# Kernel optimization log

Hardware: AMD Instinct MI355X
Metric: run time of the kernel (lower is better)

Reference implementation:

```python
import jax, jax.numpy as jnp
import numpy as np

N, D = 6144, 128
NUM_CLASSES, NUM_BATCHES = 20, 5
MIN_T, MAX_T = 0.1, 1.0
TEMP_BATCH = 0.5  # fixed per-batch-key temperature set in __init__
EPS = 1e-8        # F.cosine_similarity eps


def _class_weights(labels, n):
    c = jnp.bincount(labels, length=n).astype(jnp.float32)
    w = 1.0 / c
    return w / w.sum()


def setup_inputs() -> dict:
    key = jax.random.key(0)
    k1, k2, k3 = jax.random.split(key, 3)
    x = jax.random.normal(k1, (N, D), dtype=jnp.float32)
    targets = jax.random.randint(k2, (N,), 0, NUM_CLASSES)
    batch0 = jax.random.randint(k3, (N,), 0, NUM_BATCHES)
    return {
        "input": x,
        "temperature": jnp.float32(0.25),
        "weight_target": _class_weights(targets, NUM_CLASSES),
        "weight_batch0": _class_weights(batch0, NUM_BATCHES),
        "targets": targets,
        "batch0": batch0,
    }


def _snn_losses(S, pos_mask, neg_mask):
    # S: [N,N] exp-similarities; masks include/exclude self consistently with torch code
    diag = jnp.diagonal(S)
    pos_sum = jnp.einsum('ij,ij->i', S, pos_mask.astype(S.dtype)) - diag  # self is in pos_mask
    neg_sum = jnp.einsum('ij,ij->i', S, neg_mask.astype(S.dtype))
    cnt_pos = pos_mask.sum(axis=1)  # includes self
    cnt_neg = neg_mask.sum(axis=1)
    valid = (cnt_pos >= 2) & (cnt_neg >= 1)
    pos_safe = jnp.where(valid, pos_sum, 1.0)
    neg_safe = jnp.where(valid, neg_sum, 1.0)
    loss_i = -jnp.log(pos_safe / (pos_safe + neg_safe))
    return loss_i, valid


def _weighted_class_sum(loss_i, valid, labels, weights, num_segments):
    lsum = jax.ops.segment_sum(jnp.where(valid, loss_i, 0.0), labels, num_segments=num_segments)
    cnt = jax.ops.segment_sum(valid.astype(jnp.float32), labels, num_segments=num_segments)
    mean = lsum / jnp.maximum(cnt, 1.0)
    return jnp.sum(jnp.where(cnt > 0, mean * weights, 0.0))


def reference(input, temperature, weight_target, weight_batch0, targets, batch0):
    t = jnp.clip(temperature, MIN_T, MAX_T)
    norms = jnp.maximum(jnp.linalg.norm(input, axis=1, keepdims=True), EPS)
    xn = input / norms
    sim = xn @ xn.T  # [N, N] cosine similarity

    same_t = targets[:, None] == targets[None, :]

    # ----- target (cell-type) SNN loss -----
    S_t = jnp.exp(sim / t)
    loss_i, valid = _snn_losses(S_t, same_t, ~same_t)
    loss_target = _weighted_class_sum(loss_i, valid, targets, weight_target, NUM_CLASSES)

    # ----- batch-effect loss (one batch key), reciprocal of -log -----
    S_b = jnp.exp(sim / TEMP_BATCH)
    same_b = batch0[:, None] == batch0[None, :]
    pos_mask = same_t & same_b
    neg_mask = same_t & (~same_b)
    loss_bi, valid_b = _snn_losses(S_b, pos_mask, neg_mask)
    loss_bi = jnp.where(valid_b, 1.0 / jnp.where(valid_b, loss_bi, 1.0), 0.0)
    loss_batch = _weighted_class_sum(loss_bi, valid_b, batch0, weight_batch0, NUM_BATCHES)
    # single batch key -> mean over batch keys is just loss_batch

    return 0.9 * loss_target + 0.1 * loss_batch
```

## Files before the change

kernel.cpp:

```cpp
#include <hip/hip_runtime.h>
#include <hip/hip_bf16.h>
#include <math.h>

#define NN 6144
#define DD 128
#define NCLS 20
#define NBATCH 5
#define NB 48
#define NPAIR (NB * (NB + 1) / 2)

typedef float f32x4 __attribute__((ext_vector_type(4)));
typedef short bf16x8 __attribute__((ext_vector_type(8)));

#define SOFF (NN * DD / 2)
#define AOFF (SOFF + 4 * NN)
#define COFF (AOFF + 50)

#define GLD16(gp, lp)                                                          \
    __builtin_amdgcn_global_load_lds(                                          \
        (const __attribute__((address_space(1))) void*)(gp),                   \
        (__attribute__((address_space(3))) void*)(lp), 16, 0, 0)

__global__ __launch_bounds__(256) void k_prep(const float* __restrict__ x,
                                              float* __restrict__ ws) {
    const int t = threadIdx.x;
    if (blockIdx.x < 24) {
        float4 z = {0.f, 0.f, 0.f, 0.f};
        *(float4*)(ws + SOFF + blockIdx.x * 1024 + t * 4) = z;
    } else if (blockIdx.x == 24) {
        if (t < 51) ws[AOFF + t] = 0.0f;
    }
    const int lane = t & 63;
    const int row = blockIdx.x * 4 + (t >> 6);
    float2 v = *(const float2*)(x + row * DD + 2 * lane);
    float s = v.x * v.x + v.y * v.y;
#pragma unroll
    for (int m = 1; m < 64; m <<= 1) s += __shfl_xor(s, m, 64);
    float rinv = 1.0f / fmaxf(sqrtf(s), 1e-8f);
    __hip_bfloat16 h0 = __float2bfloat16(v.x * rinv);
    __hip_bfloat16 h1 = __float2bfloat16(v.y * rinv);
    ushort2 u;
    u.x = *(ushort*)&h0;
    u.y = *(ushort*)&h1;
    ushort* xnb = (ushort*)ws;
    *(ushort2*)(xnb + row * DD + 2 * lane) = u;
}

#define RED16(v)                                                      \
    {                                                                 \
        float s0 = up3 ? v[0] : v[2], k0 = up3 ? v[2] : v[0];         \
        float s1 = up3 ? v[1] : v[3], k1 = up3 ? v[3] : v[1];         \
        v[0] = k0 + __shfl_xor(s0, 8, 64);                            \
        v[1] = k1 + __shfl_xor(s1, 8, 64);                            \
        float s2 = up2 ? v[0] : v[1], k2 = up2 ? v[1] : v[0];         \
        v[0] = k2 + __shfl_xor(s2, 4, 64);                            \
        v[0] += __shfl_xor(v[0], 2, 64);                              \
        v[0] += __shfl_xor(v[0], 1, 64);                              \
    }

#define RED4(v)                                                       \
    {                                                                 \
        float s0 = q1 ? v[0] : v[2], k0 = q1 ? v[2] : v[0];           \
        float s1 = q1 ? v[1] : v[3], k1 = q1 ? v[3] : v[1];           \
        v[0] = k0 + __shfl_xor(s0, 32, 64);                           \
        v[1] = k1 + __shfl_xor(s1, 32, 64);                           \
        float s2 = q0 ? v[0] : v[1], k2 = q0 ? v[1] : v[0];           \
        v[0] = k2 + __shfl_xor(s2, 16, 64);                           \
    }

__global__ __launch_bounds__(256) void k_main(const float* __restrict__ temp,
                                              const int* __restrict__ tg,
                                              const int* __restrict__ bt,
                                              float* __restrict__ ws) {
    __shared__ __align__(16) char smem[32768];
    __shared__ int tgA[128], btA[128], tgB[128], btB[128];

    char* tAc = smem;
    char* tBc = smem + 16384;
    float* sRowF = (float*)smem;
    float* sColF = (float*)(smem + 4096);

    const ushort* xnb = (const ushort*)ws;
    float* PT = ws + SOFF;
    float* TT = PT + NN;
    float* PB = PT + 2 * NN;
    float* TB = PT + 3 * NN;

    int bi = 0, rem = blockIdx.x;
    while (rem >= NB - bi) { rem -= NB - bi; ++bi; }
    const int bj = bi + rem;
    const int I = bi * 128, J = bj * 128;
    const bool isDiag = (bi == bj);

    const int t = threadIdx.x;
    const int w = t >> 6;
    const int lane = t & 63;
    const int tx16 = lane & 15;
    const int quad = lane >> 4;
    const int rowBase = (w >> 1) * 64;
    const int colBase = (w & 1) * 64;

    const float tc = fminf(fmaxf(temp[0], 0.1f), 1.0f);
    const float c1 = 1.4426950408889634f / tc;
    const float c2 = 2.8853900817779268f;

    if (t < 128) { tgA[t] = tg[I + t]; btA[t] = bt[I + t]; }
    else { int u2 = t - 128; tgB[u2] = tg[J + u2]; btB[u2] = bt[J + u2]; }

    const int rloc = lane >> 3;
    const int csw = (lane & 7) ^ rloc;

    f32x4 acc[4][4];
#pragma unroll
    for (int mt = 0; mt < 4; ++mt)
#pragma unroll
        for (int nt = 0; nt < 4; ++nt) acc[mt][nt] = (f32x4){0.f, 0.f, 0.f, 0.f};

    for (int kc = 0; kc < 2; ++kc) {
        if (kc) __syncthreads();
        {
            const ushort* gA = xnb + (size_t)(I + 32 * w + rloc) * DD + kc * 64 + csw * 8;
            const ushort* gB = xnb + (size_t)(J + 32 * w + rloc) * DD + kc * 64 + csw * 8;
            char* lA = tAc + (32 * w) * 128;
            char* lB = tBc + (32 * w) * 128;
#pragma unroll
            for (int q = 0; q < 4; ++q) {
                GLD16(gA + q * 8 * DD, lA + q * 1024);
                GLD16(gB + q * 8 * DD, lB + q * 1024);
            }
        }
        __syncthreads();
#pragma unroll
        for (int ks = 0; ks < 2; ++ks) {
            bf16x8 a[4], b[4];
            const int ca = (ks * 4 + quad) ^ (tx16 & 7);
#pragma unroll
            for (int mt = 0; mt < 4; ++mt)
                a[mt] = *(const bf16x8*)(tAc + (rowBase + 16 * mt + tx16) * 128 + ca * 16);
#pragma unroll
            for (int nt = 0; nt < 4; ++nt)
                b[nt] = *(const bf16x8*)(tBc + (colBase + 16 * nt + tx16) * 128 + ca * 16);
#pragma unroll
            for (int mt = 0; mt < 4; ++mt)
#pragma unroll
                for (int nt = 0; nt < 4; ++nt)
                    acc[mt][nt] = __builtin_amdgcn_mfma_f32_16x16x32_bf16(
                        a[mt], b[nt], acc[mt][nt], 0, 0, 0);
        }
    }

    __syncthreads();

    float cPT[4] = {0}, cTT[4] = {0}, cPB[4] = {0}, cTB[4] = {0};
    int tjv[4], bjv[4];
#pragma unroll
    for (int nt = 0; nt < 4; ++nt) {
        int jl = colBase + 16 * nt + tx16;
        tjv[nt] = tgB[jl];
        bjv[nt] = btB[jl];
    }
    const bool up3 = (tx16 >> 3) & 1;
    const bool up2 = (tx16 >> 2) & 1;
    const int pOwn = tx16 >> 2;

#pragma unroll
    for (int mt = 0; mt < 4; ++mt) {
        float rPT[4] = {0}, rTT[4] = {0}, rPB[4] = {0}, rTB[4] = {0};
        int til[4], bil[4];
#pragma unroll
        for (int p = 0; p < 4; ++p) {
            int il = rowBase + 16 * mt + 4 * quad + p;
            til[p] = tgA[il];
            bil[p] = btA[il];
        }
        if (isDiag) {
#pragma unroll
            for (int nt = 0; nt < 4; ++nt) {
                const int jl = colBase + 16 * nt + tx16;
#pragma unroll
                for (int p = 0; p < 4; ++p) {
                    const int il = rowBase + 16 * mt + 4 * quad + p;
                    float s = acc[mt][nt][p];
                    float et = __builtin_amdgcn_exp2f(c1 * s);
                    float eb = __builtin_amdgcn_exp2f(c2 * s);
                    bool nd = (il != jl);
                    bool st = (til[p] == tjv[nt]) && nd;
                    bool sb = (bil[p] == bjv[nt]);
                    rTT[p] += nd ? et : 0.f;
                    rPT[p] += st ? et : 0.f;
                    rTB[p] += st ? eb : 0.f;
                    rPB[p] += (st && sb) ? eb : 0.f;
                }
            }
        } else {
#pragma unroll
            for (int nt = 0; nt < 4; ++nt) {
#pragma unroll
                for (int p = 0; p < 4; ++p) {
                    float s = acc[mt][nt][p];
                    float et = __builtin_amdgcn_exp2f(c1 * s);
                    float eb = __builtin_amdgcn_exp2f(c2 * s);
                    bool st = (til[p] == tjv[nt]);
                    bool sb = (bil[p] == bjv[nt]);
                    float etp = st ? et : 0.f;
                    float ebp = st ? eb : 0.f;
                    float ebb = (st && sb) ? eb : 0.f;
                    rTT[p] += et;
                    rPT[p] += etp;
                    rTB[p] += ebp;
                    rPB[p] += ebb;
                    cTT[nt] += et;
                    cPT[nt] += etp;
                    cTB[nt] += ebp;
                    cPB[nt] += ebb;
                }
            }
        }
        RED16(rPT);
        RED16(rTT);
        RED16(rPB);
        RED16(rTB);
        if ((tx16 & 3) == 0) {
            int il = rowBase + 16 * mt + 4 * quad + pOwn;
            int rep = (w & 1) * 512;
            sRowF[rep + 0 * 128 + il] = rPT[0];
            sRowF[rep + 1 * 128 + il] = rTT[0];
            sRowF[rep + 2 * 128 + il] = rPB[0];
            sRowF[rep + 3 * 128 + il] = rTB[0];
        }
    }
    if (!isDiag) {
        const bool q1 = (quad >> 1) & 1;
        const bool q0 = quad & 1;
        RED4(cPT);
        RED4(cTT);
        RED4(cPB);
        RED4(cTB);
        int cl = colBase + 16 * quad + tx16;
        int rep = (w >> 1) * 512;
        sColF[rep + 0 * 128 + cl] = cPT[0];
        sColF[rep + 1 * 128 + cl] = cTT[0];
        sColF[rep + 2 * 128 + cl] = cPB[0];
        sColF[rep + 3 * 128 + cl] = cTB[0];
    }

    __syncthreads();
    if (t < 128) {
        int gi = I + t;
        atomicAdd(&PT[gi], sRowF[0 * 128 + t] + sRowF[512 + 0 * 128 + t]);
        atomicAdd(&TT[gi], sRowF[1 * 128 + t] + sRowF[512 + 1 * 128 + t]);
        atomicAdd(&PB[gi], sRowF[2 * 128 + t] + sRowF[512 + 2 * 128 + t]);
        atomicAdd(&TB[gi], sRowF[3 * 128 + t] + sRowF[512 + 3 * 128 + t]);
    } else if (!isDiag) {
        int u2 = t - 128;
        int gj = J + u2;
        atomicAdd(&PT[gj], sColF[0 * 128 + u2] + sColF[512 + 0 * 128 + u2]);
        atomicAdd(&TT[gj], sColF[1 * 128 + u2] + sColF[512 + 1 * 128 + u2]);
        atomicAdd(&PB[gj], sColF[2 * 128 + u2] + sColF[512 + 2 * 128 + u2]);
        atomicAdd(&TB[gj], sColF[3 * 128 + u2] + sColF[512 + 3 * 128 + u2]);
    }
}

__global__ __launch_bounds__(256) void k_fin(const int* __restrict__ tg,
                                             const int* __restrict__ bt,
                                             const float* __restrict__ wt,
                                             const float* __restrict__ wb,
                                             float* __restrict__ ws,
                                             float* __restrict__ out) {
    __shared__ int hh[NCLS + NCLS * NBATCH];
    __shared__ float ph[4][52];
    __shared__ int lastFlag;
    const int t = threadIdx.x;
    const int wv = t >> 6;
    if (t < NCLS + NCLS * NBATCH) hh[t] = 0;
    if (t < 52 * 4) ((float*)ph)[t] = 0.0f;
    __syncthreads();
    for (int i = t; i < NN; i += 256) {
        int c = tg[i], b = bt[i];
        atomicAdd(&hh[c], 1);
        atomicAdd(&hh[NCLS + c * NBATCH + b], 1);
    }
    __syncthreads();
    const float* PT = ws + SOFF;
    const float* TT = PT + NN;
    const float* PB = PT + 2 * NN;
    const float* TB = PT + 3 * NN;
    {
        const int i = blockIdx.x * 256 + t;
        float pt = PT[i], tt = TT[i], pb = PB[i], tb = TB[i];
        int ti = tg[i], bi = bt[i];
        int cp = hh[ti];
        int cpb = hh[NCLS + ti * NBATCH + bi];
        if (cp >= 2 && (NN - cp) >= 1) {
            float loss = logf(tt / pt);
            atomicAdd(&ph[wv][ti], loss);
            atomicAdd(&ph[wv][20 + ti], 1.0f);
        }
        if (cpb >= 2 && (cp - cpb) >= 1) {
            float lb = logf(tb / pb);
            atomicAdd(&ph[wv][40 + bi], 1.0f / lb);
            atomicAdd(&ph[wv][45 + bi], 1.0f);
        }
    }
    __syncthreads();
    if (t < 50) {
        float s = ph[0][t] + ph[1][t] + ph[2][t] + ph[3][t];
        atomicAdd(&ws[AOFF + t], s);
    }
    __syncthreads();
    if (t == 0) {
        __threadfence();
        lastFlag = (atomicAdd((int*)(ws + COFF), 1) == 23) ? 1 : 0;
    }
    __syncthreads();
    if (lastFlag) {
        __threadfence();
        if (t < 64) {
            const float* acc = ws + AOFF;
            float term = 0.0f;
            if (t < NCLS) {
                float cnt = acc[NCLS + t];
                if (cnt > 0.f) term = 0.9f * (acc[t] / cnt) * wt[t];
            } else if (t >= 32 && t < 32 + NBATCH) {
                int b = t - 32;
                float cnt = acc[2 * NCLS + NBATCH + b];
                if (cnt > 0.f) term = 0.1f * (acc[2 * NCLS + b] / cnt) * wb[b];
            }
#pragma unroll
            for (int m = 1; m < 64; m <<= 1) term += __shfl_xor(term, m, 64);
            if (t == 0) out[0] = term;
        }
    }
}

extern "C" void kernel_launch(void* const* d_in, const int* in_sizes, int n_in,
                              void* d_out, int out_size, void* d_ws, size_t ws_size,
                              hipStream_t stream) {
    const float* x    = (const float*)d_in[0];
    const float* temp = (const float*)d_in[1];
    const float* wt   = (const float*)d_in[2];
    const float* wb   = (const float*)d_in[3];
    const int*   tg   = (const int*)d_in[4];
    const int*   bt   = (const int*)d_in[5];
    float* out = (float*)d_out;
    float* ws = (float*)d_ws;

    k_prep<<<NN / 4, 256, 0, stream>>>(x, ws);
    k_main<<<NPAIR, 256, 0, stream>>>(temp, tg, bt, ws);
    k_fin<<<24, 256, 0, stream>>>(tg, bt, wt, wb, ws, out);
}
```

Baseline: 99.81 us.

## Give each wave its own 64x64 triangular tile, dropping block syncs and LDS reductions

Changes the decomposition from one 128x128 upper-triangle tile per 256-thread block to one independent 64x64 tile per wave. Each wave loads its own A/B panels into a private LDS region, uses waitcnt instead of block barriers, and reads labels with wave shuffles. Row and column partial sums now go straight to global atomics, with no LDS staging. This removes block-level synchronisation and cross-wave LDS traffic. In exchange, each element of x is loaded about twice as often, global atomics increase, and LDS use per block doubles to 64KB, which may lower occupancy.

```diff
diff --git a/kernel.cpp b/kernel.cpp
--- a/kernel.cpp
+++ b/kernel.cpp
@@ -6,8 +6,8 @@
 #define DD 128
 #define NCLS 20
 #define NBATCH 5
-#define NB 48
-#define NPAIR (NB * (NB + 1) / 2)
+#define NT 96
+#define NWT (NT * (NT + 1) / 2)
 
 typedef float f32x4 __attribute__((ext_vector_type(4)));
 typedef short bf16x8 __attribute__((ext_vector_type(8)));
@@ -20,6 +20,19 @@
     __builtin_amdgcn_global_load_lds(                                          \
         (const __attribute__((address_space(1))) void*)(gp),                   \
         (__attribute__((address_space(3))) void*)(lp), 16, 0, 0)
+
+#define WAIT_VM0()                                 \
+    do {                                           \
+        __builtin_amdgcn_sched_barrier(0);         \
+        __builtin_amdgcn_s_waitcnt(0x0F70);        \
+        __builtin_amdgcn_sched_barrier(0);         \
+    } while (0)
+#define WAIT_LGKM0()                               \
+    do {                                           \
+        __builtin_amdgcn_sched_barrier(0);         \
+        __builtin_amdgcn_s_waitcnt(0xC07F);        \
+        __builtin_amdgcn_sched_barrier(0);         \
+    } while (0)
 
 __global__ __launch_bounds__(256) void k_prep(const float* __restrict__ x,
                                               float* __restrict__ ws) {
@@ -72,13 +85,7 @@
                                               const int* __restrict__ tg,
                                               const int* __restrict__ bt,
                                               float* __restrict__ ws) {
-    __shared__ __align__(16) char smem[32768];
-    __shared__ int tgA[128], btA[128], tgB[128], btB[128];
-
-    char* tAc = smem;
-    char* tBc = smem + 16384;
-    float* sRowF = (float*)smem;
-    float* sColF = (float*)(smem + 4096);
+    __shared__ __align__(16) char smem[65536];
 
     const ushort* xnb = (const ushort*)ws;
     float* PT = ws + SOFF;
@@ -86,26 +93,31 @@
     float* PB = PT + 2 * NN;
     float* TB = PT + 3 * NN;
 
-    int bi = 0, rem = blockIdx.x;
-    while (rem >= NB - bi) { rem -= NB - bi; ++bi; }
-    const int bj = bi + rem;
-    const int I = bi * 128, J = bj * 128;
-    const bool isDiag = (bi == bj);
-
     const int t = threadIdx.x;
     const int w = t >> 6;
     const int lane = t & 63;
     const int tx16 = lane & 15;
     const int quad = lane >> 4;
-    const int rowBase = (w >> 1) * 64;
-    const int colBase = (w & 1) * 64;
+
+    const int idx = blockIdx.x * 4 + w;
+    int ti = (int)((2 * NT + 1 - sqrtf((float)((2 * NT + 1) * (2 * NT + 1) - 8 * idx))) * 0.5f);
+    if (ti < 0) ti = 0;
+    if (ti > NT - 1) ti = NT - 1;
+    while (ti > 0 && ti * (2 * NT - ti + 1) / 2 > idx) --ti;
+    while ((ti + 1) * (2 * NT - ti) / 2 <= idx) ++ti;
+    const int tj = ti + (idx - ti * (2 * NT - ti + 1) / 2);
+    const int IA = ti * 64, JB = tj * 64;
+    const bool isDiag = (ti == tj);
+
+    char* lA = smem + w * 16384;
+    char* lB = lA + 8192;
 
     const float tc = fminf(fmaxf(temp[0], 0.1f), 1.0f);
     const float c1 = 1.4426950408889634f / tc;
     const float c2 = 2.8853900817779268f;
 
-    if (t < 128) { tgA[t] = tg[I + t]; btA[t] = bt[I + t]; }
-    else { int u2 = t - 128; tgB[u2] = tg[J + u2]; btB[u2] = bt[J + u2]; }
+    const int tgi = tg[IA + lane], bti = bt[IA + lane];
+    const int tgj = tg[JB + lane], btj = bt[JB + lane];
 
     const int rloc = lane >> 3;
     const int csw = (lane & 7) ^ rloc;
@@ -117,29 +129,27 @@
         for (int nt = 0; nt < 4; ++nt) acc[mt][nt] = (f32x4){0.f, 0.f, 0.f, 0.f};
 
     for (int kc = 0; kc < 2; ++kc) {
-        if (kc) __syncthreads();
+        if (kc) WAIT_LGKM0();
         {
-            const ushort* gA = xnb + (size_t)(I + 32 * w + rloc) * DD + kc * 64 + csw * 8;
-            const ushort* gB = xnb + (size_t)(J + 32 * w + rloc) * DD + kc * 64 + csw * 8;
-            char* lA = tAc + (32 * w) * 128;
-            char* lB = tBc + (32 * w) * 128;
-#pragma unroll
-            for (int q = 0; q < 4; ++q) {
-                GLD16(gA + q * 8 * DD, lA + q * 1024);
-                GLD16(gB + q * 8 * DD, lB + q * 1024);
+            const ushort* gA = xnb + (size_t)(IA + rloc) * DD + kc * 64 + csw * 8;
+            const ushort* gB = xnb + (size_t)(JB + rloc) * DD + kc * 64 + csw * 8;
+#pragma unroll
+            for (int q = 0; q < 8; ++q) {
+                GLD16(gA + (size_t)q * 8 * DD, lA + q * 1024);
+                GLD16(gB + (size_t)q * 8 * DD, lB + q * 1024);
             }
         }
-        __syncthreads();
+        WAIT_VM0();
 #pragma unroll
         for (int ks = 0; ks < 2; ++ks) {
             bf16x8 a[4], b[4];
             const int ca = (ks * 4 + quad) ^ (tx16 & 7);
 #pragma unroll
             for (int mt = 0; mt < 4; ++mt)
-                a[mt] = *(const bf16x8*)(tAc + (rowBase + 16 * mt + tx16) * 128 + ca * 16);
+                a[mt] = *(const bf16x8*)(lA + (16 * mt + tx16) * 128 + ca * 16);
 #pragma unroll
             for (int nt = 0; nt < 4; ++nt)
-                b[nt] = *(const bf16x8*)(tBc + (colBase + 16 * nt + tx16) * 128 + ca * 16);
+                b[nt] = *(const bf16x8*)(lB + (16 * nt + tx16) * 128 + ca * 16);
 #pragma unroll
             for (int mt = 0; mt < 4; ++mt)
 #pragma unroll
@@ -149,15 +159,12 @@
         }
     }
 
-    __syncthreads();
-
     float cPT[4] = {0}, cTT[4] = {0}, cPB[4] = {0}, cTB[4] = {0};
     int tjv[4], bjv[4];
 #pragma unroll
     for (int nt = 0; nt < 4; ++nt) {
-        int jl = colBase + 16 * nt + tx16;
-        tjv[nt] = tgB[jl];
-        bjv[nt] = btB[jl];
+        tjv[nt] = __shfl(tgj, 16 * nt + tx16, 64);
+        bjv[nt] = __shfl(btj, 16 * nt + tx16, 64);
     }
     const bool up3 = (tx16 >> 3) & 1;
     const bool up2 = (tx16 >> 2) & 1;
@@ -169,17 +176,16 @@
         int til[4], bil[4];
 #pragma unroll
         for (int p = 0; p < 4; ++p) {
-            int il = rowBase + 16 * mt + 4 * quad + p;
-            til[p] = tgA[il];
-            bil[p] = btA[il];
+            til[p] = __shfl(tgi, 16 * mt + 4 * quad + p, 64);
+            bil[p] = __shfl(bti, 16 * mt + 4 * quad + p, 64);
         }
         if (isDiag) {
 #pragma unroll
             for (int nt = 0; nt < 4; ++nt) {
-                const int jl = colBase + 16 * nt + tx16;
+                const int jl = 16 * nt + tx16;
 #pragma unroll
                 for (int p = 0; p < 4; ++p) {
-                    const int il = rowBase + 16 * mt + 4 * quad + p;
+                    const int il = 16 * mt + 4 * quad + p;
                     float s = acc[mt][nt][p];
                     float et = __builtin_amdgcn_exp2f(c1 * s);
                     float eb = __builtin_amdgcn_exp2f(c2 * s);
@@ -221,12 +227,11 @@
         RED16(rPB);
         RED16(rTB);
         if ((tx16 & 3) == 0) {
-            int il = rowBase + 16 * mt + 4 * quad + pOwn;
-            int rep = (w & 1) * 512;
-            sRowF[rep + 0 * 128 + il] = rPT[0];
-            sRowF[rep + 1 * 128 + il] = rTT[0];
-            sRowF[rep + 2 * 128 + il] = rPB[0];
-            sRowF[rep + 3 * 128 + il] = rTB[0];
+            int gi = IA + 16 * mt + 4 * quad + pOwn;
+            atomicAdd(&PT[gi], rPT[0]);
+            atomicAdd(&TT[gi], rTT[0]);
+            atomicAdd(&PB[gi], rPB[0]);
+            atomicAdd(&TB[gi], rTB[0]);
         }
     }
     if (!isDiag) {
@@ -236,28 +241,11 @@
         RED4(cTT);
         RED4(cPB);
         RED4(cTB);
-        int cl = colBase + 16 * quad + tx16;
-        int rep = (w >> 1) * 512;
-        sColF[rep + 0 * 128 + cl] = cPT[0];
-        sColF[rep + 1 * 128 + cl] = cTT[0];
-        sColF[rep + 2 * 128 + cl] = cPB[0];
-        sColF[rep + 3 * 128 + cl] = cTB[0];
-    }
-
-    __syncthreads();
-    if (t < 128) {
-        int gi = I + t;
-        atomicAdd(&PT[gi], sRowF[0 * 128 + t] + sRowF[512 + 0 * 128 + t]);
-        atomicAdd(&TT[gi], sRowF[1 * 128 + t] + sRowF[512 + 1 * 128 + t]);
-        atomicAdd(&PB[gi], sRowF[2 * 128 + t] + sRowF[512 + 2 * 128 + t]);
-        atomicAdd(&TB[gi], sRowF[3 * 128 + t] + sRowF[512 + 3 * 128 + t]);
-    } else if (!isDiag) {
-        int u2 = t - 128;
-        int gj = J + u2;
-        atomicAdd(&PT[gj], sColF[0 * 128 + u2] + sColF[512 + 0 * 128 + u2]);
-        atomicAdd(&TT[gj], sColF[1 * 128 + u2] + sColF[512 + 1 * 128 + u2]);
-        atomicAdd(&PB[gj], sColF[2 * 128 + u2] + sColF[512 + 2 * 128 + u2]);
-        atomicAdd(&TB[gj], sColF[3 * 128 + u2] + sColF[512 + 3 * 128 + u2]);
+        int gj = JB + 16 * quad + tx16;
+        atomicAdd(&PT[gj], cPT[0]);
+        atomicAdd(&TT[gj], cTT[0]);
+        atomicAdd(&PB[gj], cPB[0]);
+        atomicAdd(&TB[gj], cTB[0]);
     }
 }
 
@@ -346,6 +334,6 @@
     float* ws = (float*)d_ws;
 
     k_prep<<<NN / 4, 256, 0, stream>>>(x, ws);
-    k_main<<<NPAIR, 256, 0, stream>>>(temp, tg, bt, ws);
+    k_main<<<NWT / 4, 256, 0, stream>>>(temp, tg, bt, ws);
     k_fin<<<24, 256, 0, stream>>>(tg, bt, wt, wb, ws, out);
 }
```

New measurement: 102.1 us. 1.02x slower.

## Sort rows by class so cross-class tiles skip mask and positive sums

Applied to the files above, without the earlier changes.

Adds a counting sort of rows by target class in the prep kernel, writing permuted labels and original indices to workspace. The main kernel gathers rows via the sorted index, and for tile pairs whose classes cannot overlap it takes a fast path that only accumulates the total exp-sum with direct atomics, skipping label loads, mask logic and the batch-temperature exponentials. The cost is an extra O(N) histogram pass per sort block, indirect row gathers, and a branch that splits control flow.

```diff
diff --git a/kernel.cpp b/kernel.cpp
--- a/kernel.cpp
+++ b/kernel.cpp
@@ -13,7 +13,10 @@
 typedef short bf16x8 __attribute__((ext_vector_type(8)));
 
 #define SOFF (NN * DD / 2)
-#define AOFF (SOFF + 4 * NN)
+#define TGS (SOFF + 4 * NN)
+#define BTS (TGS + NN)
+#define SIO (BTS + NN)
+#define AOFF (SIO + NN)
 #define COFF (AOFF + 50)
 
 #define GLD16(gp, lp)                                                          \
@@ -22,15 +25,58 @@
         (__attribute__((address_space(3))) void*)(lp), 16, 0, 0)
 
 __global__ __launch_bounds__(256) void k_prep(const float* __restrict__ x,
+                                              const int* __restrict__ tg,
+                                              const int* __restrict__ bt,
                                               float* __restrict__ ws) {
     const int t = threadIdx.x;
+    const int lane = t & 63;
+    const int wv = t >> 6;
+    if (blockIdx.x >= 1536) {
+        __shared__ int totW[4][20], preW[4][20], ownW[4][20];
+        __shared__ int classOff[20], preC[20];
+        const int start = (blockIdx.x - 1536) * 256;
+        if (t < 240) ((int*)totW)[t < 80 ? t : t] = 0;
+        if (t < 80) { ((int*)preW)[t] = 0; ((int*)ownW)[t] = 0; }
+        __syncthreads();
+        for (int j = t; j < NN; j += 256) {
+            int cj = tg[j];
+            atomicAdd(&totW[wv][cj], 1);
+            if (j < start) atomicAdd(&preW[wv][cj], 1);
+        }
+        const int i = start + t;
+        const int c = tg[i], b = bt[i];
+        atomicAdd(&ownW[wv][c], 1);
+        __syncthreads();
+        if (t == 0) {
+            int run = 0;
+            for (int cls = 0; cls < 20; ++cls) {
+                int tot = totW[0][cls] + totW[1][cls] + totW[2][cls] + totW[3][cls];
+                classOff[cls] = run;
+                run += tot;
+            }
+        }
+        if (t < 20) preC[t] = preW[0][t] + preW[1][t] + preW[2][t] + preW[3][t];
+        __syncthreads();
+        int wb = 0;
+        for (int w2 = 0; w2 < wv; ++w2) wb += ownW[w2][c];
+        unsigned long long same = 0;
+        for (int cls = 0; cls < 20; ++cls) {
+            unsigned long long m = __ballot(c == cls);
+            if (cls == c) same = m;
+        }
+        int riw = __popcll(same & ((1ull << lane) - 1ull));
+        int rank = classOff[c] + preC[c] + wb + riw;
+        ((int*)ws)[TGS + rank] = c;
+        ((int*)ws)[BTS + rank] = b;
+        ((int*)ws)[SIO + rank] = i;
+        return;
+    }
     if (blockIdx.x < 24) {
         float4 z = {0.f, 0.f, 0.f, 0.f};
         *(float4*)(ws + SOFF + blockIdx.x * 1024 + t * 4) = z;
     } else if (blockIdx.x == 24) {
         if (t < 51) ws[AOFF + t] = 0.0f;
     }
-    const int lane = t & 63;
     const int row = blockIdx.x * 4 + (t >> 6);
     float2 v = *(const float2*)(x + row * DD + 2 * lane);
     float s = v.x * v.x + v.y * v.y;
@@ -69,8 +115,6 @@
     }
 
 __global__ __launch_bounds__(256) void k_main(const float* __restrict__ temp,
-                                              const int* __restrict__ tg,
-                                              const int* __restrict__ bt,
                                               float* __restrict__ ws) {
     __shared__ __align__(16) char smem[32768];
     __shared__ int tgA[128], btA[128], tgB[128], btB[128];
@@ -81,6 +125,9 @@
     float* sColF = (float*)(smem + 4096);
 
     const ushort* xnb = (const ushort*)ws;
+    const int* tgS = (const int*)ws + TGS;
+    const int* btS = (const int*)ws + BTS;
+    const int* sIx = (const int*)ws + SIO;
     float* PT = ws + SOFF;
     float* TT = PT + NN;
     float* PB = PT + 2 * NN;
@@ -104,9 +151,15 @@
     const float c1 = 1.4426950408889634f / tc;
     const float c2 = 2.8853900817779268f;
 
-    if (t < 128) { tgA[t] = tg[I + t]; btA[t] = bt[I + t]; }
-    else { int u2 = t - 128; tgB[u2] = tg[J + u2]; btB[u2] = bt[J + u2]; }
-
+    const bool fast = (tgS[I + 127] < tgS[J]);
+
+    if (!fast) {
+        if (t < 128) { tgA[t] = tgS[I + t]; btA[t] = btS[I + t]; }
+        else { int u2 = t - 128; tgB[u2] = tgS[J + u2]; btB[u2] = btS[J + u2]; }
+    }
+
+    const int svA = sIx[I + 32 * w + (lane & 31)];
+    const int svB = sIx[J + 32 * w + (lane & 31)];
     const int rloc = lane >> 3;
     const int csw = (lane & 7) ^ rloc;
 
@@ -119,14 +172,14 @@
     for (int kc = 0; kc < 2; ++kc) {
         if (kc) __syncthreads();
         {
-            const ushort* gA = xnb + (size_t)(I + 32 * w + rloc) * DD + kc * 64 + csw * 8;
-            const ushort* gB = xnb + (size_t)(J + 32 * w + rloc) * DD + kc * 64 + csw * 8;
             char* lA = tAc + (32 * w) * 128;
             char* lB = tBc + (32 * w) * 128;
 #pragma unroll
             for (int q = 0; q < 4; ++q) {
-                GLD16(gA + q * 8 * DD, lA + q * 1024);
-                GLD16(gB + q * 8 * DD, lB + q * 1024);
+                int rA = __shfl(svA, 8 * q + rloc, 64);
+                int rB = __shfl(svB, 8 * q + rloc, 64);
+                GLD16(xnb + (size_t)rA * DD + kc * 64 + csw * 8, lA + q * 1024);
+                GLD16(xnb + (size_t)rB * DD + kc * 64 + csw * 8, lB + q * 1024);
             }
         }
         __syncthreads();
@@ -147,6 +200,34 @@
                     acc[mt][nt] = __builtin_amdgcn_mfma_f32_16x16x32_bf16(
                         a[mt], b[nt], acc[mt][nt], 0, 0, 0);
         }
+    }
+
+    const bool up3 = (tx16 >> 3) & 1;
+    const bool up2 = (tx16 >> 2) & 1;
+    const bool q1 = (quad >> 1) & 1;
+    const bool q0 = quad & 1;
+    const int pOwn = tx16 >> 2;
+
+    if (fast) {
+        float cTT[4] = {0, 0, 0, 0};
+#pragma unroll
+        for (int mt = 0; mt < 4; ++mt) {
+            float rTT[4] = {0, 0, 0, 0};
+#pragma unroll
+            for (int nt = 0; nt < 4; ++nt)
+#pragma unroll
+                for (int p = 0; p < 4; ++p) {
+                    float et = __builtin_amdgcn_exp2f(c1 * acc[mt][nt][p]);
+                    rTT[p] += et;
+                    cTT[nt] += et;
+                }
+            RED16(rTT);
+            if ((tx16 & 3) == 0)
+                atomicAdd(&TT[I + rowBase + 16 * mt + 4 * quad + pOwn], rTT[0]);
+        }
+        RED4(cTT);
+        atomicAdd(&TT[J + colBase + 16 * quad + tx16], cTT[0]);
+        return;
     }
 
     __syncthreads();
@@ -159,9 +240,6 @@
         tjv[nt] = tgB[jl];
         bjv[nt] = btB[jl];
     }
-    const bool up3 = (tx16 >> 3) & 1;
-    const bool up2 = (tx16 >> 2) & 1;
-    const int pOwn = tx16 >> 2;
 
 #pragma unroll
     for (int mt = 0; mt < 4; ++mt) {
@@ -230,8 +308,6 @@
         }
     }
     if (!isDiag) {
-        const bool q1 = (quad >> 1) & 1;
-        const bool q0 = quad & 1;
         RED4(cPT);
         RED4(cTT);
         RED4(cPB);
@@ -285,10 +361,12 @@
     const float* TT = PT + NN;
     const float* PB = PT + 2 * NN;
     const float* TB = PT + 3 * NN;
+    const int* tgS = (const int*)ws + TGS;
+    const int* btS = (const int*)ws + BTS;
     {
         const int i = blockIdx.x * 256 + t;
         float pt = PT[i], tt = TT[i], pb = PB[i], tb = TB[i];
-        int ti = tg[i], bi = bt[i];
+        int ti = tgS[i], bi = btS[i];
         int cp = hh[ti];
         int cpb = hh[NCLS + ti * NBATCH + bi];
         if (cp >= 2 && (NN - cp) >= 1) {
@@ -345,7 +423,7 @@
     float* out = (float*)d_out;
     float* ws = (float*)d_ws;
 
-    k_prep<<<NN / 4, 256, 0, stream>>>(x, ws);
-    k_main<<<NPAIR, 256, 0, stream>>>(temp, tg, bt, ws);
+    k_prep<<<1536 + 24, 256, 0, stream>>>(x, tg, bt, ws);
+    k_main<<<NPAIR, 256, 0, stream>>>(temp, ws);
     k_fin<<<24, 256, 0, stream>>>(tg, bt, wt, wb, ws, out);
 }
```

Result: slower. 104.6 us (+4.8%).
